# Kernel optimization log

Measured on AMD Instinct MI355X. Metric: run time of the kernel, lower is better.

The kernel has to match this reference:

```python
import jax, jax.numpy as jnp
import numpy as np

DIM = 1024
SEQ = 8192
BATCH = 4
HID = 128
TARGET_RATIO = 0.5
MIN_SEQ_LEN = 2048


def setup_inputs() -> dict:
    key = jax.random.key(0)
    k0, k1, k2, k3, k4 = jax.random.split(key, 5)
    x = jax.random.normal(k0, (BATCH, SEQ, DIM), dtype=jnp.float32)
    # torch.nn.Linear default init: U(-1/sqrt(fan_in), 1/sqrt(fan_in))
    s1 = 1.0 / np.sqrt(DIM)
    s2 = 1.0 / np.sqrt(HID)
    W1 = jax.random.uniform(k1, (DIM, HID), jnp.float32, -s1, s1)
    b1 = jax.random.uniform(k2, (HID,), jnp.float32, -s1, s1)
    W2 = jax.random.uniform(k3, (HID, 1), jnp.float32, -s2, s2)
    b2 = jax.random.uniform(k4, (1,), jnp.float32, -s2, s2)
    return {"x": x, "W1": W1, "b1": b1, "W2": W2, "b2": b2}


def reference(x, W1, b1, W2, b2):
    B, S, D = x.shape
    # importance scorer: Linear -> GELU (exact, matching torch nn.GELU) -> Linear, squeeze(-1)
    h = jax.nn.gelu(jnp.einsum('bsd,dh->bsh', x, W1) + b1, approximate=False)
    scores = (jnp.einsum('bsh,ho->bso', h, W2) + b2)[..., 0]  # [B, S]

    # keep_ratio = max(0.1, target_ratio * min(1, min_seq_len / seq_len))
    length_factor = min(1.0, MIN_SEQ_LEN / S)
    keep_ratio = max(0.1, TARGET_RATIO * length_factor)
    num_keep = max(1, int(S * keep_ratio))  # static at trace time

    _, indices = jax.lax.top_k(scores, num_keep)       # [B, num_keep]
    indices = jnp.sort(indices, axis=1)                # restore temporal order
    kept_tokens = jnp.take_along_axis(x, indices[..., None], axis=1)  # [B, num_keep, D]
    return kept_tokens, indices
```

## Files before the change

### kernel.cpp

```cpp
#include <hip/hip_runtime.h>
#include <hip/hip_bf16.h>

#define DIMD 1024
#define HIDD 128
#define SEQ  8192
#define BATCH 4
#define KEEP 1024

typedef __attribute__((ext_vector_type(8))) short short8;
typedef __attribute__((ext_vector_type(4))) float f32x4;
typedef __attribute__((ext_vector_type(4))) unsigned int u32x4;

__device__ __forceinline__ unsigned short f2bf(float f) {
    unsigned u = __float_as_uint(f);
    u += 0x7FFFu + ((u >> 16) & 1u);
    return (unsigned short)(u >> 16);
}
__device__ __forceinline__ float bf2f(unsigned short h) {
    return __uint_as_float((unsigned)h << 16);
}
__device__ __forceinline__ float gelu_exact(float h) {
    return 0.5f * h * (1.0f + erff(h * 0.70710678118654752440f));
}
__device__ __forceinline__ void gload_lds16(const void* g, void* l) {
    __builtin_amdgcn_global_load_lds(
        (const __attribute__((address_space(1))) void*)g,
        (__attribute__((address_space(3))) void*)l, 16, 0, 0);
}

__global__ __launch_bounds__(256)
void w1split_kernel(const float* __restrict__ W1, char* __restrict__ img) {
    const int t = blockIdx.x * 256 + threadIdx.x;
    const int c = t & 127;
    const int j = (t >> 7) & 7;
    const int kt = t >> 10;
    u32x4 ph, pm, pl;
    unsigned short hs[8], ms[8], ls[8];
#pragma unroll
    for (int i = 0; i < 8; ++i) {
        const float f = W1[(kt * 64 + j * 8 + i) * 128 + c];
        const unsigned short h = f2bf(f);  const float r1 = f - bf2f(h);
        const unsigned short m = f2bf(r1); const float r2 = r1 - bf2f(m);
        const unsigned short l = f2bf(r2);
        hs[i] = h; ms[i] = m; ls[i] = l;
    }
#pragma unroll
    for (int p = 0; p < 4; ++p) {
        ph[p] = (unsigned)hs[2 * p] | ((unsigned)hs[2 * p + 1] << 16);
        pm[p] = (unsigned)ms[2 * p] | ((unsigned)ms[2 * p + 1] << 16);
        pl[p] = (unsigned)ls[2 * p] | ((unsigned)ls[2 * p + 1] << 16);
    }
    const int off = kt * 16384 + c * 128 + 16 * (j ^ (c & 7));
    *(u32x4*)(img + 0 * 262144 + off) = ph;
    *(u32x4*)(img + 1 * 262144 + off) = pm;
    *(u32x4*)(img + 2 * 262144 + off) = pl;
}

__global__ __launch_bounds__(256, 2)
void score_mfma(const float* __restrict__ x, const char* __restrict__ w1img,
                const float* __restrict__ b1, const float* __restrict__ W2,
                const float* __restrict__ b2, float* __restrict__ scores) {
    __shared__ __align__(16) char lds[73728];
    char* const Abuf[3] = { lds, lds + 8192, lds + 16384 };
    char* const Bbuf[3] = { lds + 24576, lds + 40960, lds + 57344 };

    const int tid = threadIdx.x;
    const int lane = tid & 63;
    const int wid = tid >> 6;
    const int wm = wid >> 1;
    const int wn = wid & 1;
    const long rowBase = (long)blockIdx.x * 64;

    f32x4 acc[2][4];
#pragma unroll
    for (int m = 0; m < 2; ++m)
#pragma unroll
        for (int n = 0; n < 4; ++n) acc[m][n] = (f32x4){0.f, 0.f, 0.f, 0.f};

    for (int kt = 0; kt < DIMD; kt += 64) {
        __syncthreads();
        {
            const long tbase = (long)(kt >> 6) * 16384;
#pragma unroll
            for (int limb = 0; limb < 3; ++limb)
#pragma unroll
                for (int i = 0; i < 4; ++i) {
                    const int off = wid * 4096 + i * 1024;
                    gload_lds16(w1img + (long)limb * 262144 + tbase + off + lane * 16,
                                Bbuf[limb] + off);
                }
        }
        {
            const int row = tid >> 2, q = tid & 3;
            const float* gx = x + (rowBase + row) * DIMD + kt + q * 16;
#pragma unroll
            for (int j = 0; j < 2; ++j) {
                const f32x4 v0 = *(const f32x4*)(gx + j * 8);
                const f32x4 v1 = *(const f32x4*)(gx + j * 8 + 4);
                float va[8];
#pragma unroll
                for (int i = 0; i < 4; ++i) { va[i] = v0[i]; va[4 + i] = v1[i]; }
                u32x4 qh, qm, ql;
#pragma unroll
                for (int p = 0; p < 4; ++p) {
                    const float f0 = va[2 * p], f1 = va[2 * p + 1];
                    const unsigned short h0 = f2bf(f0);  const float r10 = f0 - bf2f(h0);
                    const unsigned short m0 = f2bf(r10); const float r20 = r10 - bf2f(m0);
                    const unsigned short l0 = f2bf(r20);
                    const unsigned short h1 = f2bf(f1);  const float r11 = f1 - bf2f(h1);
                    const unsigned short m1 = f2bf(r11); const float r21 = r11 - bf2f(m1);
                    const unsigned short l1 = f2bf(r21);
                    qh[p] = (unsigned)h0 | ((unsigned)h1 << 16);
                    qm[p] = (unsigned)m0 | ((unsigned)m1 << 16);
                    ql[p] = (unsigned)l0 | ((unsigned)l1 << 16);
                }
                const int kb = q * 32 + j * 16;
                const int off = row * 128 + (kb ^ ((row & 7) << 4));
                *(u32x4*)(Abuf[0] + off) = qh;
                *(u32x4*)(Abuf[1] + off) = qm;
                *(u32x4*)(Abuf[2] + off) = ql;
            }
        }
        __syncthreads();

#pragma unroll
        for (int ks = 0; ks < 2; ++ks) {
            const int kbase = ks * 64 + (lane >> 4) * 16;
            short8 bh[4], bm[4], bl[4];
#pragma unroll
            for (int n = 0; n < 4; ++n) {
                const int col = wn * 64 + n * 16 + (lane & 15);
                const int off = col * 128 + (kbase ^ ((col & 7) << 4));
                bh[n] = *(const short8*)(Bbuf[0] + off);
                bm[n] = *(const short8*)(Bbuf[1] + off);
                bl[n] = *(const short8*)(Bbuf[2] + off);
            }
#pragma unroll
            for (int m = 0; m < 2; ++m) {
                const int row = wm * 32 + m * 16 + (lane & 15);
                const int off = row * 128 + (kbase ^ ((row & 7) << 4));
                const short8 ah = *(const short8*)(Abuf[0] + off);
                const short8 am = *(const short8*)(Abuf[1] + off);
                const short8 al = *(const short8*)(Abuf[2] + off);
#pragma unroll
                for (int n = 0; n < 4; ++n) {
                    acc[m][n] = __builtin_amdgcn_mfma_f32_16x16x32_bf16(ah, bh[n], acc[m][n], 0, 0, 0);
                    acc[m][n] = __builtin_amdgcn_mfma_f32_16x16x32_bf16(ah, bm[n], acc[m][n], 0, 0, 0);
                    acc[m][n] = __builtin_amdgcn_mfma_f32_16x16x32_bf16(am, bh[n], acc[m][n], 0, 0, 0);
                    acc[m][n] = __builtin_amdgcn_mfma_f32_16x16x32_bf16(am, bm[n], acc[m][n], 0, 0, 0);
                    acc[m][n] = __builtin_amdgcn_mfma_f32_16x16x32_bf16(ah, bl[n], acc[m][n], 0, 0, 0);
                    acc[m][n] = __builtin_amdgcn_mfma_f32_16x16x32_bf16(al, bh[n], acc[m][n], 0, 0, 0);
                }
            }
        }
    }

    float rsum[2][4];
#pragma unroll
    for (int m = 0; m < 2; ++m)
#pragma unroll
        for (int r = 0; r < 4; ++r) rsum[m][r] = 0.f;
#pragma unroll
    for (int n = 0; n < 4; ++n) {
        const int col = wn * 64 + n * 16 + (lane & 15);
        const float b1c = b1[col], w2c = W2[col];
#pragma unroll
        for (int m = 0; m < 2; ++m)
#pragma unroll
            for (int r = 0; r < 4; ++r)
                rsum[m][r] += gelu_exact(acc[m][n][r] + b1c) * w2c;
    }
#pragma unroll
    for (int m = 0; m < 2; ++m)
#pragma unroll
        for (int r = 0; r < 4; ++r) {
#pragma unroll
            for (int o = 1; o < 16; o <<= 1)
                rsum[m][r] += __shfl_xor(rsum[m][r], o, 64);
        }
    __syncthreads();
    float* scpad = (float*)lds;
    if ((lane & 15) == 0) {
#pragma unroll
        for (int m = 0; m < 2; ++m)
#pragma unroll
            for (int r = 0; r < 4; ++r) {
                const int row = wm * 32 + m * 16 + (lane >> 4) * 4 + r;
                scpad[wn * 64 + row] = rsum[m][r];
            }
    }
    __syncthreads();
    if (tid < 64)
        scores[rowBase + tid] = scpad[tid] + scpad[64 + tid] + b2[0];
}

__device__ __forceinline__ unsigned sortable_u32(float f) {
    unsigned u = __float_as_uint(f);
    return (u & 0x80000000u) ? ~u : (u | 0x80000000u);
}

__global__ __launch_bounds__(1024)
void select_kernel(const float* __restrict__ scores, int* __restrict__ idx_out,
                   float* __restrict__ out_tail) {
    const int b = blockIdx.x;
    const int t = threadIdx.x;
    const int wave = t >> 6, lane = t & 63;

    __shared__ unsigned wh[16 * 256];
    __shared__ unsigned wsum[16];
    __shared__ unsigned sbc_bin, sbc_sub;

    unsigned key[8];
    {
        const float* sc = scores + b * SEQ + t * 8;
        f32x4 v0 = *(const f32x4*)(sc);
        f32x4 v1 = *(const f32x4*)(sc + 4);
#pragma unroll
        for (int i = 0; i < 4; ++i) {
            key[i] = sortable_u32(v0[i]);
            key[4 + i] = sortable_u32(v1[i]);
        }
    }

    unsigned prefix = 0, need = KEEP;
    for (int r = 0; r < 4; ++r) {
        const int shift = 24 - 8 * r;
        const unsigned mask_hi = (r == 0) ? 0u : (0xFFFFFFFFu << (shift + 8));
#pragma unroll
        for (int i = 0; i < 4; ++i) wh[t + i * 1024] = 0;
        __syncthreads();
#pragma unroll
        for (int j = 0; j < 8; ++j)
            if ((key[j] & mask_hi) == prefix)
                atomicAdd(&wh[wave * 256 + ((key[j] >> shift) & 255u)], 1u);
        __syncthreads();
        if (t < 256) {
            unsigned s = 0;
#pragma unroll
            for (int w = 0; w < 16; ++w) s += wh[w * 256 + t];
            wh[t] = s;
        }
        __syncthreads();
        if (wave == 0) {
            const unsigned h0 = wh[lane * 4 + 0], h1 = wh[lane * 4 + 1];
            const unsigned h2 = wh[lane * 4 + 2], h3 = wh[lane * 4 + 3];
            const unsigned s3 = h3, s2 = h2 + s3, s1 = h1 + s2, s0 = h0 + s1;
            unsigned run = s0;
#pragma unroll
            for (int d = 1; d < 64; d <<= 1) {
                const unsigned v = __shfl_down(run, d, 64);
                if (lane + d < 64) run += v;
            }
            const unsigned above = run - s0;
            const unsigned suf0 = above + s0, suf1 = above + s1;
            const unsigned suf2 = above + s2, suf3 = above + s3;
            if (suf1 < need && need <= suf0) { sbc_bin = lane * 4 + 0; sbc_sub = suf1; }
            if (suf2 < need && need <= suf1) { sbc_bin = lane * 4 + 1; sbc_sub = suf2; }
            if (suf3 < need && need <= suf2) { sbc_bin = lane * 4 + 2; sbc_sub = suf3; }
            if (above < need && need <= suf3) { sbc_bin = lane * 4 + 3; sbc_sub = above; }
        }
        __syncthreads();
        prefix |= sbc_bin << shift;
        need -= sbc_sub;
        __syncthreads();
    }
    const unsigned tau = prefix;
    const unsigned m = need;

    unsigned pk[8], tsum = 0;
#pragma unroll
    for (int j = 0; j < 8; ++j) {
        const unsigned gt = (key[j] > tau) ? 1u : 0u;
        const unsigned eq = (key[j] == tau) ? 1u : 0u;
        pk[j] = tsum;
        tsum += (gt << 16) | eq;
    }
    unsigned incl = tsum;
#pragma unroll
    for (int d = 1; d < 64; d <<= 1) {
        const unsigned v = __shfl_up(incl, d, 64);
        if (lane >= d) incl += v;
    }
    if (lane == 63) wsum[wave] = incl;
    __syncthreads();
    if (t == 0) {
        unsigned run = 0;
        for (int w = 0; w < 16; ++w) { const unsigned tmp = wsum[w]; wsum[w] = run; run += tmp; }
    }
    __syncthreads();
    const unsigned base = wsum[wave] + (incl - tsum);

#pragma unroll
    for (int j = 0; j < 8; ++j) {
        const unsigned before = base + pk[j];
        const unsigned gt_before = before >> 16;
        const unsigned eq_before = before & 0xFFFFu;
        const bool keep = (key[j] > tau) || (key[j] == tau && eq_before < m);
        if (keep) {
            const unsigned pos = gt_before + (eq_before < m ? eq_before : m);
            const int idx = t * 8 + j;
            idx_out[b * KEEP + pos] = idx;
            out_tail[b * KEEP + pos] = (float)idx;
        }
    }
}

__global__ __launch_bounds__(256)
void gather_kernel(const float* __restrict__ x, const int* __restrict__ idx,
                   float* __restrict__ out) {
    const int j = blockIdx.x;
    const int b = j >> 10;
    const int id = idx[j];
    const f32x4* src = (const f32x4*)(x + ((long)b * SEQ + id) * DIMD);
    f32x4* dst = (f32x4*)(out + (long)j * DIMD);
    dst[threadIdx.x] = src[threadIdx.x];
}

extern "C" void kernel_launch(void* const* d_in, const int* in_sizes, int n_in,
                              void* d_out, int out_size, void* d_ws, size_t ws_size,
                              hipStream_t stream) {
    const float* x  = (const float*)d_in[0];
    const float* W1 = (const float*)d_in[1];
    const float* b1 = (const float*)d_in[2];
    const float* W2 = (const float*)d_in[3];
    const float* b2 = (const float*)d_in[4];
    float* out = (float*)d_out;

    char* ws = (char*)d_ws;
    char*  w1img  = ws;
    float* scores = (float*)(ws + 786432);
    int*   idxbuf = (int*)(ws + 786432 + 131072);

    w1split_kernel<<<64, 256, 0, stream>>>(W1, w1img);
    score_mfma<<<(BATCH * SEQ) / 64, 256, 0, stream>>>(x, w1img, b1, W2, b2, scores);
    select_kernel<<<BATCH, 1024, 0, stream>>>(scores, idxbuf,
                                              out + (long)BATCH * KEEP * DIMD);
    gather_kernel<<<BATCH * KEEP, 256, 0, stream>>>(x, idxbuf, out);
}
```

Measured before the change: 241.0 us.

## Replace 3-limb bf16 split GEMM with 2-limb scaled fp16 split

The fp32 scorer GEMM was emulated with three bf16 limbs and six MFMAs per tile. It now uses two fp16 limbs, the low limb scaled by 4096, and three MFMAs, with the cross terms kept in a separate accumulator and rescaled in the epilogue. This halves MFMA work and cuts LDS and conversion traffic, and the smaller LDS footprint allows launch bounds of 3 blocks per CU. The risks are lower accuracy near the top-k score boundary, and fp16 range or underflow problems for large or tiny values.

```diff
diff --git a/kernel.cpp b/kernel.cpp
--- a/kernel.cpp
+++ b/kernel.cpp
@@ -8,17 +8,10 @@
 #define KEEP 1024
 
 typedef __attribute__((ext_vector_type(8))) short short8;
+typedef __attribute__((ext_vector_type(8))) _Float16 f16x8;
 typedef __attribute__((ext_vector_type(4))) float f32x4;
 typedef __attribute__((ext_vector_type(4))) unsigned int u32x4;
 
-__device__ __forceinline__ unsigned short f2bf(float f) {
-    unsigned u = __float_as_uint(f);
-    u += 0x7FFFu + ((u >> 16) & 1u);
-    return (unsigned short)(u >> 16);
-}
-__device__ __forceinline__ float bf2f(unsigned short h) {
-    return __uint_as_float((unsigned)h << 16);
-}
 __device__ __forceinline__ float gelu_exact(float h) {
     return 0.5f * h * (1.0f + erff(h * 0.70710678118654752440f));
 }
@@ -34,35 +27,28 @@
     const int c = t & 127;
     const int j = (t >> 7) & 7;
     const int kt = t >> 10;
-    u32x4 ph, pm, pl;
-    unsigned short hs[8], ms[8], ls[8];
+    f16x8 hv, lv;
 #pragma unroll
     for (int i = 0; i < 8; ++i) {
         const float f = W1[(kt * 64 + j * 8 + i) * 128 + c];
-        const unsigned short h = f2bf(f);  const float r1 = f - bf2f(h);
-        const unsigned short m = f2bf(r1); const float r2 = r1 - bf2f(m);
-        const unsigned short l = f2bf(r2);
-        hs[i] = h; ms[i] = m; ls[i] = l;
-    }
-#pragma unroll
-    for (int p = 0; p < 4; ++p) {
-        ph[p] = (unsigned)hs[2 * p] | ((unsigned)hs[2 * p + 1] << 16);
-        pm[p] = (unsigned)ms[2 * p] | ((unsigned)ms[2 * p + 1] << 16);
-        pl[p] = (unsigned)ls[2 * p] | ((unsigned)ls[2 * p + 1] << 16);
+        const _Float16 h = (_Float16)f;
+        const _Float16 l = (_Float16)((f - (float)h) * 4096.0f);
+        hv[i] = h; lv[i] = l;
     }
     const int off = kt * 16384 + c * 128 + 16 * (j ^ (c & 7));
-    *(u32x4*)(img + 0 * 262144 + off) = ph;
-    *(u32x4*)(img + 1 * 262144 + off) = pm;
-    *(u32x4*)(img + 2 * 262144 + off) = pl;
-}
-
-__global__ __launch_bounds__(256, 2)
+    *(f16x8*)(img + off) = hv;
+    *(f16x8*)(img + 262144 + off) = lv;
+}
+
+__global__ __launch_bounds__(256, 3)
 void score_mfma(const float* __restrict__ x, const char* __restrict__ w1img,
                 const float* __restrict__ b1, const float* __restrict__ W2,
                 const float* __restrict__ b2, float* __restrict__ scores) {
-    __shared__ __align__(16) char lds[73728];
-    char* const Abuf[3] = { lds, lds + 8192, lds + 16384 };
-    char* const Bbuf[3] = { lds + 24576, lds + 40960, lds + 57344 };
+    __shared__ __align__(16) char lds[49152];
+    char* const Ah = lds;
+    char* const Al = lds + 8192;
+    char* const Bh = lds + 16384;
+    char* const Bl = lds + 32768;
 
     const int tid = threadIdx.x;
     const int lane = tid & 63;
@@ -71,24 +57,25 @@
     const int wn = wid & 1;
     const long rowBase = (long)blockIdx.x * 64;
 
-    f32x4 acc[2][4];
+    f32x4 acc[2][4], acc2[2][4];
 #pragma unroll
     for (int m = 0; m < 2; ++m)
 #pragma unroll
-        for (int n = 0; n < 4; ++n) acc[m][n] = (f32x4){0.f, 0.f, 0.f, 0.f};
+        for (int n = 0; n < 4; ++n) {
+            acc[m][n] = (f32x4){0.f, 0.f, 0.f, 0.f};
+            acc2[m][n] = (f32x4){0.f, 0.f, 0.f, 0.f};
+        }
 
     for (int kt = 0; kt < DIMD; kt += 64) {
         __syncthreads();
         {
             const long tbase = (long)(kt >> 6) * 16384;
 #pragma unroll
-            for (int limb = 0; limb < 3; ++limb)
-#pragma unroll
-                for (int i = 0; i < 4; ++i) {
-                    const int off = wid * 4096 + i * 1024;
-                    gload_lds16(w1img + (long)limb * 262144 + tbase + off + lane * 16,
-                                Bbuf[limb] + off);
-                }
+            for (int i = 0; i < 4; ++i) {
+                const int off = wid * 4096 + i * 1024;
+                gload_lds16(w1img + tbase + off + lane * 16, Bh + off);
+                gload_lds16(w1img + 262144 + tbase + off + lane * 16, Bl + off);
+            }
         }
         {
             const int row = tid >> 2, q = tid & 3;
@@ -97,28 +84,19 @@
             for (int j = 0; j < 2; ++j) {
                 const f32x4 v0 = *(const f32x4*)(gx + j * 8);
                 const f32x4 v1 = *(const f32x4*)(gx + j * 8 + 4);
-                float va[8];
-#pragma unroll
-                for (int i = 0; i < 4; ++i) { va[i] = v0[i]; va[4 + i] = v1[i]; }
-                u32x4 qh, qm, ql;
-#pragma unroll
-                for (int p = 0; p < 4; ++p) {
-                    const float f0 = va[2 * p], f1 = va[2 * p + 1];
-                    const unsigned short h0 = f2bf(f0);  const float r10 = f0 - bf2f(h0);
-                    const unsigned short m0 = f2bf(r10); const float r20 = r10 - bf2f(m0);
-                    const unsigned short l0 = f2bf(r20);
-                    const unsigned short h1 = f2bf(f1);  const float r11 = f1 - bf2f(h1);
-                    const unsigned short m1 = f2bf(r11); const float r21 = r11 - bf2f(m1);
-                    const unsigned short l1 = f2bf(r21);
-                    qh[p] = (unsigned)h0 | ((unsigned)h1 << 16);
-                    qm[p] = (unsigned)m0 | ((unsigned)m1 << 16);
-                    ql[p] = (unsigned)l0 | ((unsigned)l1 << 16);
+                f16x8 hv, lv;
+#pragma unroll
+                for (int i = 0; i < 4; ++i) {
+                    const _Float16 h0 = (_Float16)v0[i];
+                    const _Float16 h1 = (_Float16)v1[i];
+                    hv[i] = h0; hv[4 + i] = h1;
+                    lv[i] = (_Float16)((v0[i] - (float)h0) * 4096.0f);
+                    lv[4 + i] = (_Float16)((v1[i] - (float)h1) * 4096.0f);
                 }
                 const int kb = q * 32 + j * 16;
                 const int off = row * 128 + (kb ^ ((row & 7) << 4));
-                *(u32x4*)(Abuf[0] + off) = qh;
-                *(u32x4*)(Abuf[1] + off) = qm;
-                *(u32x4*)(Abuf[2] + off) = ql;
+                *(f16x8*)(Ah + off) = hv;
+                *(f16x8*)(Al + off) = lv;
             }
         }
         __syncthreads();
@@ -126,30 +104,25 @@
 #pragma unroll
         for (int ks = 0; ks < 2; ++ks) {
             const int kbase = ks * 64 + (lane >> 4) * 16;
-            short8 bh[4], bm[4], bl[4];
+            f16x8 ah[2], al[2];
+#pragma unroll
+            for (int m = 0; m < 2; ++m) {
+                const int row = wm * 32 + m * 16 + (lane & 15);
+                const int off = row * 128 + (kbase ^ ((row & 7) << 4));
+                ah[m] = *(const f16x8*)(Ah + off);
+                al[m] = *(const f16x8*)(Al + off);
+            }
 #pragma unroll
             for (int n = 0; n < 4; ++n) {
                 const int col = wn * 64 + n * 16 + (lane & 15);
                 const int off = col * 128 + (kbase ^ ((col & 7) << 4));
-                bh[n] = *(const short8*)(Bbuf[0] + off);
-                bm[n] = *(const short8*)(Bbuf[1] + off);
-                bl[n] = *(const short8*)(Bbuf[2] + off);
-            }
-#pragma unroll
-            for (int m = 0; m < 2; ++m) {
-                const int row = wm * 32 + m * 16 + (lane & 15);
-                const int off = row * 128 + (kbase ^ ((row & 7) << 4));
-                const short8 ah = *(const short8*)(Abuf[0] + off);
-                const short8 am = *(const short8*)(Abuf[1] + off);
-                const short8 al = *(const short8*)(Abuf[2] + off);
-#pragma unroll
-                for (int n = 0; n < 4; ++n) {
-                    acc[m][n] = __builtin_amdgcn_mfma_f32_16x16x32_bf16(ah, bh[n], acc[m][n], 0, 0, 0);
-                    acc[m][n] = __builtin_amdgcn_mfma_f32_16x16x32_bf16(ah, bm[n], acc[m][n], 0, 0, 0);
-                    acc[m][n] = __builtin_amdgcn_mfma_f32_16x16x32_bf16(am, bh[n], acc[m][n], 0, 0, 0);
-                    acc[m][n] = __builtin_amdgcn_mfma_f32_16x16x32_bf16(am, bm[n], acc[m][n], 0, 0, 0);
-                    acc[m][n] = __builtin_amdgcn_mfma_f32_16x16x32_bf16(ah, bl[n], acc[m][n], 0, 0, 0);
-                    acc[m][n] = __builtin_amdgcn_mfma_f32_16x16x32_bf16(al, bh[n], acc[m][n], 0, 0, 0);
+                const f16x8 bh = *(const f16x8*)(Bh + off);
+                const f16x8 bl = *(const f16x8*)(Bl + off);
+#pragma unroll
+                for (int m = 0; m < 2; ++m) {
+                    acc[m][n]  = __builtin_amdgcn_mfma_f32_16x16x32_f16(ah[m], bh, acc[m][n], 0, 0, 0);
+                    acc2[m][n] = __builtin_amdgcn_mfma_f32_16x16x32_f16(ah[m], bl, acc2[m][n], 0, 0, 0);
+                    acc2[m][n] = __builtin_amdgcn_mfma_f32_16x16x32_f16(al[m], bh, acc2[m][n], 0, 0, 0);
                 }
             }
         }
@@ -167,8 +140,10 @@
 #pragma unroll
         for (int m = 0; m < 2; ++m)
 #pragma unroll
-            for (int r = 0; r < 4; ++r)
-                rsum[m][r] += gelu_exact(acc[m][n][r] + b1c) * w2c;
+            for (int r = 0; r < 4; ++r) {
+                const float h = acc[m][n][r] + 2.44140625e-4f * acc2[m][n][r] + b1c;
+                rsum[m][r] += gelu_exact(h) * w2c;
+            }
     }
 #pragma unroll
     for (int m = 0; m < 2; ++m)
@@ -328,8 +303,8 @@
 
     char* ws = (char*)d_ws;
     char*  w1img  = ws;
-    float* scores = (float*)(ws + 786432);
-    int*   idxbuf = (int*)(ws + 786432 + 131072);
+    float* scores = (float*)(ws + 524288);
+    int*   idxbuf = (int*)(ws + 524288 + 131072);
 
     w1split_kernel<<<64, 256, 0, stream>>>(W1, w1img);
     score_mfma<<<(BATCH * SEQ) / 64, 256, 0, stream>>>(x, w1img, b1, W2, b2, scores);
```

Measured after the change: 229.7 us. 1.05x faster.
